# Performance work log

Hardware: AMD Instinct MI355X
Metric: run time of the kernel (lower is better)

Reference implementation:

```python
import jax, jax.numpy as jnp
import numpy as np

VOCAB, EMB, RNN, OUT = 32000, 512, 1024, 4


def setup_inputs() -> dict:
    key = jax.random.key(0)
    ks = jax.random.split(key, 8)
    stdv = 1.0 / np.sqrt(RNN)
    u = lambda k, shape, s: jax.random.uniform(k, shape, jnp.float32, -s, s)
    return {
        "x": jax.random.randint(ks[0], (512, 64), 0, VOCAB),
        "emb_table": jax.random.normal(ks[1], (VOCAB, EMB), jnp.float32),
        "w_ih": u(ks[2], (3 * RNN, EMB), stdv),
        "w_hh": u(ks[3], (3 * RNN, RNN), stdv),
        "b_ih": u(ks[4], (3 * RNN,), stdv),
        "b_hh": u(ks[5], (3 * RNN,), stdv),
        "fc_w": u(ks[6], (OUT, RNN), 1.0 / np.sqrt(RNN)),
        "fc_b": u(ks[7], (OUT,), 1.0 / np.sqrt(RNN)),
    }


def reference(x, emb_table, w_ih, w_hh, b_ih, b_hh, fc_w, fc_b):
    # x: [T, B] int indices
    T, B = x.shape
    embedded = emb_table[x]  # [T, B, EMB]
    # precompute input projections for all timesteps at once: [T, B, 3*RNN]
    gi_all = jnp.einsum('tbe,ge->tbg', embedded, w_ih) + b_ih

    def step(h, gi):
        gh = h @ w_hh.T + b_hh  # [B, 3*RNN]
        i_r, i_i, i_n = jnp.split(gi, 3, axis=1)
        h_r, h_i, h_n = jnp.split(gh, 3, axis=1)
        r = jax.nn.sigmoid(i_r + h_r)
        z = jax.nn.sigmoid(i_i + h_i)
        n = jnp.tanh(i_n + r * h_n)
        hy = z * n + (1.0 - z) * h  # note: matches GRUCellExposed (z gates newgate)
        return hy, hy

    h0 = jnp.zeros((B, w_hh.shape[1]), embedded.dtype)
    h_last, _ = jax.lax.scan(step, h0, gi_all)
    out = h_last @ fc_w.T + fc_b  # [B, OUT]
    return out
```

## Files before the change

### kernel.cpp

```cpp
#include <hip/hip_runtime.h>
#include <hip/hip_bf16.h>

typedef __attribute__((ext_vector_type(8))) short  short8;
typedef __attribute__((ext_vector_type(4))) float  f32x4;

#define T_TOTAL 512
#define BATCH   64
#define EMB     512
#define RNN     1024
#define G3      3072
#define WROWS   48
#define WPAD    1032
#define RPAD    18
#define NWG     256
#define NGRP    4
#define NLINE   2
#define SMEM_BYTES (WROWS * WPAD * 2 + 4 * WROWS * RPAD * 4)

__device__ __forceinline__ unsigned short f2bf(float f) {
    union { float f; unsigned int u; } v; v.f = f;
    unsigned int r = v.u + 0x7fffu + ((v.u >> 16) & 1u);
    return (unsigned short)(r >> 16);
}
__device__ __forceinline__ float bf2f(unsigned short h) {
    union { unsigned int u; float f; } v; v.u = ((unsigned int)h) << 16;
    return v.f;
}
__device__ __forceinline__ float sigmoidf_(float x) { return 1.f / (1.f + __expf(-x)); }
__device__ __forceinline__ float tanhf_(float x) {
    float ax = fabsf(x);
    float e2 = __expf(-2.f * ax);
    float t  = (1.f - e2) / (1.f + e2);
    return x < 0.f ? -t : t;
}

__device__ __forceinline__ void gbar_arrive(unsigned int* lines, int lid,
                                            unsigned int ph) {
    __syncthreads();
    if (threadIdx.x == 0)
        __hip_atomic_fetch_add(&lines[lid * 64], 1u,
                               __ATOMIC_RELAXED, __HIP_MEMORY_SCOPE_AGENT);
}
__device__ __forceinline__ void gbar_wait(unsigned int* lines, unsigned int ph) {
    if (threadIdx.x < NLINE) {
        while (__hip_atomic_load(&lines[threadIdx.x * 64], __ATOMIC_RELAXED,
                                 __HIP_MEMORY_SCOPE_AGENT) < ph * 32u)
            __builtin_amdgcn_s_sleep(1);
    }
    __syncthreads();
}

__global__ void bar_init(unsigned int* bar) {
    for (int i = threadIdx.x; i < NGRP * 256; i += 256) bar[i] = 0;
}

__global__ __launch_bounds__(256) void gi_kernel(
    const int* __restrict__ x, const float* __restrict__ emb,
    const float* __restrict__ w_ih, const float* __restrict__ b_ih,
    unsigned short* __restrict__ gi, int t0)
{
    __shared__ __align__(16) unsigned short Asm[128 * 40];
    __shared__ __align__(16) unsigned short Bsm[128 * 40];

    const int tid = threadIdx.x;
    const int m0 = blockIdx.x * 128;
    const int n0 = blockIdx.y * 128;

    const int r    = tid >> 1;
    const int half = tid & 1;
    const int xi = x[t0 * BATCH + m0 + r];
    const float* arow = emb  + (size_t)xi * EMB + half * 16;
    const float* brow = w_ih + (size_t)(n0 + r) * EMB + half * 16;
    unsigned short* adst = &Asm[r * 40 + half * 16];
    unsigned short* bdst = &Bsm[r * 40 + half * 16];

    const int lane = tid & 63, wv = tid >> 6;
    const int m_off = (wv & 1) * 64, n_off = (wv >> 1) * 64;
    const int lr = lane & 15, lq = lane >> 4;

    f32x4 acc[4][4];
    #pragma unroll
    for (int i = 0; i < 4; ++i)
        #pragma unroll
        for (int j = 0; j < 4; ++j) acc[i][j] = (f32x4){0.f, 0.f, 0.f, 0.f};

    for (int k0 = 0; k0 < EMB; k0 += 32) {
        const float4 a0 = *(const float4*)(arow + k0);
        const float4 a1 = *(const float4*)(arow + k0 + 4);
        const float4 a2 = *(const float4*)(arow + k0 + 8);
        const float4 a3 = *(const float4*)(arow + k0 + 12);
        const float4 b0 = *(const float4*)(brow + k0);
        const float4 b1 = *(const float4*)(brow + k0 + 4);
        const float4 b2 = *(const float4*)(brow + k0 + 8);
        const float4 b3 = *(const float4*)(brow + k0 + 12);
        __syncthreads();
        short8 av0, av1, bv0, bv1;
        av0[0]=f2bf(a0.x); av0[1]=f2bf(a0.y); av0[2]=f2bf(a0.z); av0[3]=f2bf(a0.w);
        av0[4]=f2bf(a1.x); av0[5]=f2bf(a1.y); av0[6]=f2bf(a1.z); av0[7]=f2bf(a1.w);
        av1[0]=f2bf(a2.x); av1[1]=f2bf(a2.y); av1[2]=f2bf(a2.z); av1[3]=f2bf(a2.w);
        av1[4]=f2bf(a3.x); av1[5]=f2bf(a3.y); av1[6]=f2bf(a3.z); av1[7]=f2bf(a3.w);
        bv0[0]=f2bf(b0.x); bv0[1]=f2bf(b0.y); bv0[2]=f2bf(b0.z); bv0[3]=f2bf(b0.w);
        bv0[4]=f2bf(b1.x); bv0[5]=f2bf(b1.y); bv0[6]=f2bf(b1.z); bv0[7]=f2bf(b1.w);
        bv1[0]=f2bf(b2.x); bv1[1]=f2bf(b2.y); bv1[2]=f2bf(b2.z); bv1[3]=f2bf(b2.w);
        bv1[4]=f2bf(b3.x); bv1[5]=f2bf(b3.y); bv1[6]=f2bf(b3.z); bv1[7]=f2bf(b3.w);
        *(short8*)(adst)     = av0;
        *(short8*)(adst + 8) = av1;
        *(short8*)(bdst)     = bv0;
        *(short8*)(bdst + 8) = bv1;
        __syncthreads();

        short8 fa[4], fb[4];
        #pragma unroll
        for (int i = 0; i < 4; ++i) {
            fa[i] = *(const short8*)&Asm[(m_off + i * 16 + lr) * 40 + lq * 8];
            fb[i] = *(const short8*)&Bsm[(n_off + i * 16 + lr) * 40 + lq * 8];
        }
        #pragma unroll
        for (int mi = 0; mi < 4; ++mi)
            #pragma unroll
            for (int ni = 0; ni < 4; ++ni)
                acc[mi][ni] = __builtin_amdgcn_mfma_f32_16x16x32_bf16(
                    fa[mi], fb[ni], acc[mi][ni], 0, 0, 0);
    }

    float bia[4];
    #pragma unroll
    for (int ni = 0; ni < 4; ++ni) bia[ni] = b_ih[n0 + n_off + ni * 16 + lr];
    #pragma unroll
    for (int mi = 0; mi < 4; ++mi)
        #pragma unroll
        for (int ni = 0; ni < 4; ++ni) {
            const int n = n0 + n_off + ni * 16 + lr;
            #pragma unroll
            for (int q = 0; q < 4; ++q) {
                const int m = m0 + m_off + mi * 16 + lq * 4 + q;
                gi[(size_t)m * G3 + n] = f2bf(acc[mi][ni][q] + bia[ni]);
            }
        }
}

__global__ __launch_bounds__(256, 1) void rec_kernel(
    const unsigned short* __restrict__ gi,
    const float* __restrict__ w_hh, const float* __restrict__ b_hh,
    unsigned short* __restrict__ hb0, unsigned short* __restrict__ hb1,
    float* __restrict__ hf, unsigned int* bar, int t0, int nsteps, int pbase)
{
    extern __shared__ __align__(16) char smem[];
    unsigned short* Wsm = (unsigned short*)smem;
    float (*red)[WROWS][RPAD] = (float (*)[WROWS][RPAD])(smem + WROWS * WPAD * 2);

    const int tid = threadIdx.x;
    const int wg  = blockIdx.x;
    const int grp = wg & 3, sidx = wg >> 2;
    const int b0 = grp * 16, j0 = sidx * 16;
    unsigned int* lines = &bar[grp * 256];
    const int lid = sidx & (NLINE - 1);

    #pragma unroll 4
    for (int it = 0; it < 48; ++it) {
        const int i   = it * 256 + tid;
        const int row = i >> 8;
        const int c4  = (i & 255) * 4;
        const int gate = row >> 4, uu = row & 15;
        const float4 v = *(const float4*)(w_hh + (size_t)(gate * RNN + j0 + uu) * RNN + c4);
        unsigned short* dst = &Wsm[row * WPAD + c4];
        dst[0] = f2bf(v.x); dst[1] = f2bf(v.y); dst[2] = f2bf(v.z); dst[3] = f2bf(v.w);
    }

    const int u  = tid & 15;
    const int bl = tid >> 4;
    const int j  = j0 + u;
    const int b  = b0 + bl;
    const float bhr = b_hh[j], bhi = b_hh[RNN + j], bhn = b_hh[2 * RNN + j];

    float h_reg;
    if (t0 == 0) {
        h_reg = 0.f;
        if ((u & 1) == 0)
            __hip_atomic_store((unsigned int*)&hb0[b * RNN + j], 0u,
                               __ATOMIC_RELAXED, __HIP_MEMORY_SCOPE_AGENT);
    } else {
        h_reg = hf[b * RNN + j];
    }
    gbar_arrive(lines, lid, (unsigned)(pbase + 1));

    size_t gb = (size_t)b * G3 + j0 + u;
    float gir = bf2f(gi[gb]);
    float gii = bf2f(gi[gb + RNN]);
    float gin = bf2f(gi[gb + 2 * RNN]);
    gbar_wait(lines, (unsigned)(pbase + 1));

    const int lane = tid & 63, kq = tid >> 6;
    const int lr = lane & 15, lq = lane >> 4;
    const unsigned short* wbase = Wsm + kq * 256 + lq * 8;
    const size_t hoff = ((size_t)(b0 + lr) * RNN + kq * 256 + lq * 8) >> 2;

    for (int t = 0; t < nsteps; ++t) {
        const unsigned short* hrd = (t & 1) ? hb1 : hb0;
        unsigned short*       hwr = (t & 1) ? hb0 : hb1;

        union { unsigned long long q[2]; short8 s8; } hv[8];
        const unsigned long long* hp = (const unsigned long long*)hrd + hoff;
        #pragma unroll
        for (int ks = 0; ks < 8; ++ks) {
            hv[ks].q[0] = __hip_atomic_load(hp + ks * 8,     __ATOMIC_RELAXED,
                                            __HIP_MEMORY_SCOPE_AGENT);
            hv[ks].q[1] = __hip_atomic_load(hp + ks * 8 + 1, __ATOMIC_RELAXED,
                                            __HIP_MEMORY_SCOPE_AGENT);
        }

        f32x4 acc[3];
        acc[0] = (f32x4){0.f, 0.f, 0.f, 0.f};
        acc[1] = (f32x4){0.f, 0.f, 0.f, 0.f};
        acc[2] = (f32x4){0.f, 0.f, 0.f, 0.f};
        #pragma unroll
        for (int ks = 0; ks < 8; ++ks) {
            const int k = ks * 32;
            #pragma unroll
            for (int gt = 0; gt < 3; ++gt) {
                const short8 a = *(const short8*)(wbase + (gt * 16 + lr) * WPAD + k);
                acc[gt] = __builtin_amdgcn_mfma_f32_16x16x32_bf16(a, hv[ks].s8,
                                                                  acc[gt], 0, 0, 0);
            }
        }
        #pragma unroll
        for (int gt = 0; gt < 3; ++gt)
            #pragma unroll
            for (int q = 0; q < 4; ++q)
                red[kq][gt * 16 + lq * 4 + q][lr] = acc[gt][q];
        __syncthreads();

        const float ghr = red[0][u][bl]      + red[1][u][bl]
                        + red[2][u][bl]      + red[3][u][bl];
        const float ghi = red[0][16 + u][bl] + red[1][16 + u][bl]
                        + red[2][16 + u][bl] + red[3][16 + u][bl];
        const float ghn = red[0][32 + u][bl] + red[1][32 + u][bl]
                        + red[2][32 + u][bl] + red[3][32 + u][bl];
        const float rr = sigmoidf_(gir + ghr + bhr);
        const float zz = sigmoidf_(gii + ghi + bhi);
        const float nn = tanhf_(gin + rr * (ghn + bhn));
        h_reg = zz * nn + (1.f - zz) * h_reg;

        unsigned int hvv = (unsigned int)f2bf(h_reg);
        unsigned int ovv = __shfl_xor((int)hvv, 1);
        if ((u & 1) == 0)
            __hip_atomic_store((unsigned int*)&hwr[b * RNN + j],
                               hvv | (ovv << 16), __ATOMIC_RELAXED,
                               __HIP_MEMORY_SCOPE_AGENT);

        gbar_arrive(lines, lid, (unsigned)(pbase + 2 + t));
        const int tn = (t + 1 < nsteps) ? t + 1 : t;
        gb = ((size_t)tn * BATCH + b) * G3 + j0 + u;
        const float ngr = bf2f(gi[gb]);
        const float ngi = bf2f(gi[gb + RNN]);
        const float ngn = bf2f(gi[gb + 2 * RNN]);
        gbar_wait(lines, (unsigned)(pbase + 2 + t));
        gir = ngr; gii = ngi; gin = ngn;
    }
    hf[b * RNN + j] = h_reg;
}

__global__ __launch_bounds__(256) void out_kernel(
    const float* __restrict__ hf, const float* __restrict__ fc_w,
    const float* __restrict__ fc_b, float* __restrict__ out)
{
    __shared__ float red[256];
    const int bidx = blockIdx.x, tid = threadIdx.x;
    const int o = tid & 3, seg = tid >> 2;
    const float* hp = hf   + (size_t)bidx * RNN + seg * 16;
    const float* wp = fc_w + (size_t)o * RNN + seg * 16;
    float acc = 0.f;
    #pragma unroll
    for (int i = 0; i < 16; ++i) acc += hp[i] * wp[i];
    red[tid] = acc;
    __syncthreads();
    if (tid < 4) {
        float sv = fc_b[tid];
        #pragma unroll 8
        for (int q = 0; q < 64; ++q) sv += red[q * 4 + tid];
        out[bidx * 4 + tid] = sv;
    }
}

extern "C" void kernel_launch(void* const* d_in, const int* in_sizes, int n_in,
                              void* d_out, int out_size, void* d_ws, size_t ws_size,
                              hipStream_t stream)
{
    const int*   x     = (const int*)d_in[0];
    const float* emb   = (const float*)d_in[1];
    const float* w_ih  = (const float*)d_in[2];
    const float* w_hh  = (const float*)d_in[3];
    const float* b_ih  = (const float*)d_in[4];
    const float* b_hh  = (const float*)d_in[5];
    const float* fc_w  = (const float*)d_in[6];
    const float* fc_b  = (const float*)d_in[7];
    float*       out   = (float*)d_out;

    const size_t aux = 2 * (size_t)BATCH * RNN * 2 + (size_t)BATCH * RNN * 4
                     + NGRP * 256 * 4;
    const int tch  = (ws_size >= (size_t)T_TOTAL * BATCH * G3 * 2 + aux) ? 512 : 128;
    const int nchk = T_TOTAL / tch;

    char* ws = (char*)d_ws;
    unsigned short* gi_buf = (unsigned short*)ws;
    size_t off = (size_t)tch * BATCH * G3 * 2;
    unsigned short* hb0 = (unsigned short*)(ws + off); off += (size_t)BATCH * RNN * 2;
    unsigned short* hb1 = (unsigned short*)(ws + off); off += (size_t)BATCH * RNN * 2;
    float*          hf  = (float*)(ws + off);          off += (size_t)BATCH * RNN * 4;
    unsigned int*   bar = (unsigned int*)(ws + off);

    hipFuncSetAttribute((const void*)rec_kernel,
                        hipFuncAttributeMaxDynamicSharedMemorySize, SMEM_BYTES);

    bar_init<<<dim3(1), dim3(256), 0, stream>>>(bar);

    for (int c = 0; c < nchk; ++c) {
        int t0 = c * tch, ns = tch, pb = c * (tch + 1);
        gi_kernel<<<dim3(tch * BATCH / 128, 24), dim3(256), 0, stream>>>(
            x, emb, w_ih, b_ih, gi_buf, t0);
        void* args[10];
        args[0] = (void*)&gi_buf; args[1] = (void*)&w_hh; args[2] = (void*)&b_hh;
        args[3] = (void*)&hb0;    args[4] = (void*)&hb1;  args[5] = (void*)&hf;
        args[6] = (void*)&bar;    args[7] = (void*)&t0;   args[8] = (void*)&ns;
        args[9] = (void*)&pb;
        hipLaunchCooperativeKernel((const void*)rec_kernel, dim3(NWG), dim3(256),
                                   args, SMEM_BYTES, stream);
    }
    out_kernel<<<dim3(BATCH), dim3(256), 0, stream>>>(hf, fc_w, fc_b, out);
}
```

Baseline: 2.130 ms.

## Replace per-step grid barrier with epoch-tagged hidden-state flags polled by consumers

Removes the atomic counter barrier between timesteps. Each hidden value is now stored as a 32-bit word whose upper half holds an epoch/step tag, and consumers spin on the exact h slices they need until every tag matches. This is meant to cut global barrier latency and let workgroups proceed as soon as their dependencies are ready. The reduction buffer is double-buffered so the lack of a trailing syncthreads stays safe. The cost is doubled h buffer traffic, inline-asm cache-bypassing loads, and a persistent epoch counter that must not wrap.

Result: slower. 3.000 ms (+40.9%).

```diff
diff --git a/kernel.cpp b/kernel.cpp
--- a/kernel.cpp
+++ b/kernel.cpp
@@ -3,6 +3,7 @@
 
 typedef __attribute__((ext_vector_type(8))) short  short8;
 typedef __attribute__((ext_vector_type(4))) float  f32x4;
+typedef __attribute__((ext_vector_type(4))) unsigned int u32x4;
 
 #define T_TOTAL 512
 #define BATCH   64
@@ -13,9 +14,7 @@
 #define WPAD    1032
 #define RPAD    18
 #define NWG     256
-#define NGRP    4
-#define NLINE   2
-#define SMEM_BYTES (WROWS * WPAD * 2 + 4 * WROWS * RPAD * 4)
+#define SMEM_BYTES (WROWS * WPAD * 2 + 2 * 4 * WROWS * RPAD * 4)
 
 __device__ __forceinline__ unsigned short f2bf(float f) {
     union { float f; unsigned int u; } v; v.f = f;
@@ -34,25 +33,7 @@
     return x < 0.f ? -t : t;
 }
 
-__device__ __forceinline__ void gbar_arrive(unsigned int* lines, int lid,
-                                            unsigned int ph) {
-    __syncthreads();
-    if (threadIdx.x == 0)
-        __hip_atomic_fetch_add(&lines[lid * 64], 1u,
-                               __ATOMIC_RELAXED, __HIP_MEMORY_SCOPE_AGENT);
-}
-__device__ __forceinline__ void gbar_wait(unsigned int* lines, unsigned int ph) {
-    if (threadIdx.x < NLINE) {
-        while (__hip_atomic_load(&lines[threadIdx.x * 64], __ATOMIC_RELAXED,
-                                 __HIP_MEMORY_SCOPE_AGENT) < ph * 32u)
-            __builtin_amdgcn_s_sleep(1);
-    }
-    __syncthreads();
-}
-
-__global__ void bar_init(unsigned int* bar) {
-    for (int i = threadIdx.x; i < NGRP * 256; i += 256) bar[i] = 0;
-}
+__global__ void epoch_kernel(unsigned int* ep) { if (threadIdx.x == 0) ++*ep; }
 
 __global__ __launch_bounds__(256) void gi_kernel(
     const int* __restrict__ x, const float* __restrict__ emb,
@@ -142,19 +123,21 @@
 __global__ __launch_bounds__(256, 1) void rec_kernel(
     const unsigned short* __restrict__ gi,
     const float* __restrict__ w_hh, const float* __restrict__ b_hh,
-    unsigned short* __restrict__ hb0, unsigned short* __restrict__ hb1,
-    float* __restrict__ hf, unsigned int* bar, int t0, int nsteps, int pbase)
+    unsigned int* __restrict__ hb0, unsigned int* __restrict__ hb1,
+    float* __restrict__ hf, const unsigned int* __restrict__ ep,
+    int t0, int nsteps)
 {
     extern __shared__ __align__(16) char smem[];
     unsigned short* Wsm = (unsigned short*)smem;
-    float (*red)[WROWS][RPAD] = (float (*)[WROWS][RPAD])(smem + WROWS * WPAD * 2);
+    float (*red)[4][WROWS][RPAD] =
+        (float (*)[4][WROWS][RPAD])(smem + WROWS * WPAD * 2);
 
     const int tid = threadIdx.x;
     const int wg  = blockIdx.x;
     const int grp = wg & 3, sidx = wg >> 2;
     const int b0 = grp * 16, j0 = sidx * 16;
-    unsigned int* lines = &bar[grp * 256];
-    const int lid = sidx & (NLINE - 1);
+
+    const unsigned int ebase = ep[0] * 1024u;
 
     #pragma unroll 4
     for (int it = 0; it < 48; ++it) {
@@ -176,37 +159,80 @@
     float h_reg;
     if (t0 == 0) {
         h_reg = 0.f;
-        if ((u & 1) == 0)
-            __hip_atomic_store((unsigned int*)&hb0[b * RNN + j], 0u,
-                               __ATOMIC_RELAXED, __HIP_MEMORY_SCOPE_AGENT);
+        __hip_atomic_store(&hb0[(size_t)b * RNN + j], ebase << 16,
+                           __ATOMIC_RELAXED, __HIP_MEMORY_SCOPE_AGENT);
     } else {
-        h_reg = hf[b * RNN + j];
-    }
-    gbar_arrive(lines, lid, (unsigned)(pbase + 1));
-
-    size_t gb = (size_t)b * G3 + j0 + u;
-    float gir = bf2f(gi[gb]);
-    float gii = bf2f(gi[gb + RNN]);
-    float gin = bf2f(gi[gb + 2 * RNN]);
-    gbar_wait(lines, (unsigned)(pbase + 1));
+        h_reg = hf[(size_t)b * RNN + j];
+    }
+    __syncthreads();
+
+    {
+    }
+    size_t gb0 = (size_t)b * G3 + j;
+    float gir = bf2f(gi[gb0]);
+    float gii = bf2f(gi[gb0 + RNN]);
+    float gin = bf2f(gi[gb0 + 2 * RNN]);
 
     const int lane = tid & 63, kq = tid >> 6;
     const int lr = lane & 15, lq = lane >> 4;
     const unsigned short* wbase = Wsm + kq * 256 + lq * 8;
-    const size_t hoff = ((size_t)(b0 + lr) * RNN + kq * 256 + lq * 8) >> 2;
+    const unsigned int* hpo0 = hb0 + (size_t)(b0 + lr) * RNN + kq * 256 + lq * 8;
+    const unsigned int* hpo1 = hb1 + (size_t)(b0 + lr) * RNN + kq * 256 + lq * 8;
+    unsigned int* hw0 = hb0 + (size_t)b * RNN + j;
+    unsigned int* hw1 = hb1 + (size_t)b * RNN + j;
 
     for (int t = 0; t < nsteps; ++t) {
-        const unsigned short* hrd = (t & 1) ? hb1 : hb0;
-        unsigned short*       hwr = (t & 1) ? hb0 : hb1;
-
-        union { unsigned long long q[2]; short8 s8; } hv[8];
-        const unsigned long long* hp = (const unsigned long long*)hrd + hoff;
+        const int g = t0 + t;
+        const unsigned int texp = (ebase + (unsigned)g) << 16;
+        const unsigned int* hp = (g & 1) ? hpo1 : hpo0;
+        unsigned int* hwp      = (g & 1) ? hw0  : hw1;
+
+        const int tn = (t + 1 < nsteps) ? t + 1 : t;
+        const size_t gbn = ((size_t)tn * BATCH + b) * G3 + j;
+        const float ngr = bf2f(gi[gbn]);
+        const float ngi = bf2f(gi[gbn + RNN]);
+        const float ngn = bf2f(gi[gbn + 2 * RNN]);
+
+        for (;;) {
+            unsigned int s = 0;
+            #pragma unroll
+            for (int ks = 0; ks < 8; ++ks)
+                s |= __hip_atomic_load(hp + ks * 32, __ATOMIC_RELAXED,
+                                       __HIP_MEMORY_SCOPE_AGENT) ^ texp;
+            if (__all((s & 0xFFFF0000u) == 0)) break;
+        }
+
+        u32x4 q0[8], q1[8];
+        for (;;) {
+            #pragma unroll
+            for (int ks = 0; ks < 8; ++ks) {
+                asm volatile("global_load_dwordx4 %0, %1, off sc0 sc1"
+                             : "=v"(q0[ks]) : "v"(hp + ks * 32) : "memory");
+                asm volatile("global_load_dwordx4 %0, %1, off sc0 sc1"
+                             : "=v"(q1[ks]) : "v"(hp + ks * 32 + 4) : "memory");
+            }
+            asm volatile("s_waitcnt vmcnt(0)" ::: "memory");
+            __builtin_amdgcn_sched_barrier(0);
+            unsigned int s = 0;
+            #pragma unroll
+            for (int ks = 0; ks < 8; ++ks) {
+                s |= (q0[ks].x ^ texp) | (q0[ks].y ^ texp)
+                   | (q0[ks].z ^ texp) | (q0[ks].w ^ texp);
+                s |= (q1[ks].x ^ texp) | (q1[ks].y ^ texp)
+                   | (q1[ks].z ^ texp) | (q1[ks].w ^ texp);
+            }
+            if (__all((s & 0xFFFF0000u) == 0)) break;
+        }
+
+        short8 hfrag[8];
         #pragma unroll
         for (int ks = 0; ks < 8; ++ks) {
-            hv[ks].q[0] = __hip_atomic_load(hp + ks * 8,     __ATOMIC_RELAXED,
-                                            __HIP_MEMORY_SCOPE_AGENT);
-            hv[ks].q[1] = __hip_atomic_load(hp + ks * 8 + 1, __ATOMIC_RELAXED,
-                                            __HIP_MEMORY_SCOPE_AGENT);
+            union { unsigned int d[4]; short8 s8; } pk;
+            pk.d[0] = __builtin_amdgcn_perm(q0[ks].y, q0[ks].x, 0x05040100u);
+            pk.d[1] = __builtin_amdgcn_perm(q0[ks].w, q0[ks].z, 0x05040100u);
+            pk.d[2] = __builtin_amdgcn_perm(q1[ks].y, q1[ks].x, 0x05040100u);
+            pk.d[3] = __builtin_amdgcn_perm(q1[ks].w, q1[ks].z, 0x05040100u);
+            hfrag[ks] = pk.s8;
         }
 
         f32x4 acc[3];
@@ -219,45 +245,34 @@
             #pragma unroll
             for (int gt = 0; gt < 3; ++gt) {
                 const short8 a = *(const short8*)(wbase + (gt * 16 + lr) * WPAD + k);
-                acc[gt] = __builtin_amdgcn_mfma_f32_16x16x32_bf16(a, hv[ks].s8,
+                acc[gt] = __builtin_amdgcn_mfma_f32_16x16x32_bf16(a, hfrag[ks],
                                                                   acc[gt], 0, 0, 0);
             }
         }
+        float (*rcur)[WROWS][RPAD] = red[t & 1];
         #pragma unroll
         for (int gt = 0; gt < 3; ++gt)
             #pragma unroll
             for (int q = 0; q < 4; ++q)
-                red[kq][gt * 16 + lq * 4 + q][lr] = acc[gt][q];
+                rcur[kq][gt * 16 + lq * 4 + q][lr] = acc[gt][q];
         __syncthreads();
 
-        const float ghr = red[0][u][bl]      + red[1][u][bl]
-                        + red[2][u][bl]      + red[3][u][bl];
-        const float ghi = red[0][16 + u][bl] + red[1][16 + u][bl]
-                        + red[2][16 + u][bl] + red[3][16 + u][bl];
-        const float ghn = red[0][32 + u][bl] + red[1][32 + u][bl]
-                        + red[2][32 + u][bl] + red[3][32 + u][bl];
+        const float ghr = rcur[0][u][bl]      + rcur[1][u][bl]
+                        + rcur[2][u][bl]      + rcur[3][u][bl];
+        const float ghi = rcur[0][16 + u][bl] + rcur[1][16 + u][bl]
+                        + rcur[2][16 + u][bl] + rcur[3][16 + u][bl];
+        const float ghn = rcur[0][32 + u][bl] + rcur[1][32 + u][bl]
+                        + rcur[2][32 + u][bl] + rcur[3][32 + u][bl];
         const float rr = sigmoidf_(gir + ghr + bhr);
         const float zz = sigmoidf_(gii + ghi + bhi);
         const float nn = tanhf_(gin + rr * (ghn + bhn));
         h_reg = zz * nn + (1.f - zz) * h_reg;
 
-        unsigned int hvv = (unsigned int)f2bf(h_reg);
-        unsigned int ovv = __shfl_xor((int)hvv, 1);
-        if ((u & 1) == 0)
-            __hip_atomic_store((unsigned int*)&hwr[b * RNN + j],
-                               hvv | (ovv << 16), __ATOMIC_RELAXED,
-                               __HIP_MEMORY_SCOPE_AGENT);
-
-        gbar_arrive(lines, lid, (unsigned)(pbase + 2 + t));
-        const int tn = (t + 1 < nsteps) ? t + 1 : t;
-        gb = ((size_t)tn * BATCH + b) * G3 + j0 + u;
-        const float ngr = bf2f(gi[gb]);
-        const float ngi = bf2f(gi[gb + RNN]);
-        const float ngn = bf2f(gi[gb + 2 * RNN]);
-        gbar_wait(lines, (unsigned)(pbase + 2 + t));
+        __hip_atomic_store(hwp, (texp + 0x10000u) | (unsigned)f2bf(h_reg),
+                           __ATOMIC_RELAXED, __HIP_MEMORY_SCOPE_AGENT);
         gir = ngr; gii = ngi; gin = ngn;
     }
-    hf[b * RNN + j] = h_reg;
+    hf[(size_t)b * RNN + j] = h_reg;
 }
 
 __global__ __launch_bounds__(256) void out_kernel(
@@ -296,33 +311,31 @@
     const float* fc_b  = (const float*)d_in[7];
     float*       out   = (float*)d_out;
 
-    const size_t aux = 2 * (size_t)BATCH * RNN * 2 + (size_t)BATCH * RNN * 4
-                     + NGRP * 256 * 4;
+    const size_t aux = 3 * (size_t)BATCH * RNN * 4 + 256;
     const int tch  = (ws_size >= (size_t)T_TOTAL * BATCH * G3 * 2 + aux) ? 512 : 128;
     const int nchk = T_TOTAL / tch;
 
     char* ws = (char*)d_ws;
     unsigned short* gi_buf = (unsigned short*)ws;
     size_t off = (size_t)tch * BATCH * G3 * 2;
-    unsigned short* hb0 = (unsigned short*)(ws + off); off += (size_t)BATCH * RNN * 2;
-    unsigned short* hb1 = (unsigned short*)(ws + off); off += (size_t)BATCH * RNN * 2;
-    float*          hf  = (float*)(ws + off);          off += (size_t)BATCH * RNN * 4;
-    unsigned int*   bar = (unsigned int*)(ws + off);
+    unsigned int* hb0 = (unsigned int*)(ws + off); off += (size_t)BATCH * RNN * 4;
+    unsigned int* hb1 = (unsigned int*)(ws + off); off += (size_t)BATCH * RNN * 4;
+    float*        hf  = (float*)(ws + off);        off += (size_t)BATCH * RNN * 4;
+    unsigned int* ep  = (unsigned int*)(ws + off);
 
     hipFuncSetAttribute((const void*)rec_kernel,
                         hipFuncAttributeMaxDynamicSharedMemorySize, SMEM_BYTES);
 
-    bar_init<<<dim3(1), dim3(256), 0, stream>>>(bar);
+    epoch_kernel<<<dim3(1), dim3(1), 0, stream>>>(ep);
 
     for (int c = 0; c < nchk; ++c) {
-        int t0 = c * tch, ns = tch, pb = c * (tch + 1);
+        int t0 = c * tch, ns = tch;
         gi_kernel<<<dim3(tch * BATCH / 128, 24), dim3(256), 0, stream>>>(
             x, emb, w_ih, b_ih, gi_buf, t0);
-        void* args[10];
+        void* args[9];
         args[0] = (void*)&gi_buf; args[1] = (void*)&w_hh; args[2] = (void*)&b_hh;
         args[3] = (void*)&hb0;    args[4] = (void*)&hb1;  args[5] = (void*)&hf;
-        args[6] = (void*)&bar;    args[7] = (void*)&t0;   args[8] = (void*)&ns;
-        args[9] = (void*)&pb;
+        args[6] = (void*)&ep;     args[7] = (void*)&t0;   args[8] = (void*)&ns;
         hipLaunchCooperativeKernel((const void*)rec_kernel, dim3(NWG), dim3(256),
                                    args, SMEM_BYTES, stream);
     }
```

## Split grid barrier into per-k-quarter lines and pre-convert GEMM inputs to bf16

Applied to the files above, without the earlier changes.

The recurrent kernel's group barrier changes from two shared counters, which every block waited on, to four counters indexed by the block's j-quarter. Each wave polls only the counter for the quarter of h it reads, and waves proceed independently without a block-wide syncthreads after the wait, which should shorten the per-step barrier latency. Separately, when workspace allows, the embedding table and w_ih are converted to bf16 up front so the input-projection GEMM loads half the bytes and skips per-tile conversion. The cost is converting the whole 32000x512 embedding table, most of which is never gathered, and the per-wave waits add memory-ordering risk.

New measurement: 2.286 ms. +7.3%, slower.

```diff
diff --git a/kernel.cpp b/kernel.cpp
--- a/kernel.cpp
+++ b/kernel.cpp
@@ -6,6 +6,7 @@
 
 #define T_TOTAL 512
 #define BATCH   64
+#define VOCAB   32000
 #define EMB     512
 #define RNN     1024
 #define G3      3072
@@ -14,7 +15,7 @@
 #define RPAD    18
 #define NWG     256
 #define NGRP    4
-#define NLINE   2
+#define NLINE   4
 #define SMEM_BYTES (WROWS * WPAD * 2 + 4 * WROWS * RPAD * 4)
 
 __device__ __forceinline__ unsigned short f2bf(float f) {
@@ -34,29 +35,27 @@
     return x < 0.f ? -t : t;
 }
 
-__device__ __forceinline__ void gbar_arrive(unsigned int* lines, int lid,
-                                            unsigned int ph) {
-    __syncthreads();
-    if (threadIdx.x == 0)
-        __hip_atomic_fetch_add(&lines[lid * 64], 1u,
-                               __ATOMIC_RELAXED, __HIP_MEMORY_SCOPE_AGENT);
-}
-__device__ __forceinline__ void gbar_wait(unsigned int* lines, unsigned int ph) {
-    if (threadIdx.x < NLINE) {
-        while (__hip_atomic_load(&lines[threadIdx.x * 64], __ATOMIC_RELAXED,
-                                 __HIP_MEMORY_SCOPE_AGENT) < ph * 32u)
-            __builtin_amdgcn_s_sleep(1);
-    }
-    __syncthreads();
-}
-
 __global__ void bar_init(unsigned int* bar) {
     for (int i = threadIdx.x; i < NGRP * 256; i += 256) bar[i] = 0;
 }
 
+__global__ __launch_bounds__(256) void cvt_bf16_kernel(
+    const float* __restrict__ s, unsigned short* __restrict__ d, int n8)
+{
+    const int i = blockIdx.x * 256 + threadIdx.x;
+    if (i >= n8) return;
+    const float4 a = ((const float4*)s)[i * 2];
+    const float4 b = ((const float4*)s)[i * 2 + 1];
+    short8 v;
+    v[0] = f2bf(a.x); v[1] = f2bf(a.y); v[2] = f2bf(a.z); v[3] = f2bf(a.w);
+    v[4] = f2bf(b.x); v[5] = f2bf(b.y); v[6] = f2bf(b.z); v[7] = f2bf(b.w);
+    ((short8*)d)[i] = v;
+}
+
+template<bool BF>
 __global__ __launch_bounds__(256) void gi_kernel(
-    const int* __restrict__ x, const float* __restrict__ emb,
-    const float* __restrict__ w_ih, const float* __restrict__ b_ih,
+    const int* __restrict__ x, const void* __restrict__ embp,
+    const void* __restrict__ wihp, const float* __restrict__ b_ih,
     unsigned short* __restrict__ gi, int t0)
 {
     __shared__ __align__(16) unsigned short Asm[128 * 40];
@@ -69,8 +68,6 @@
     const int r    = tid >> 1;
     const int half = tid & 1;
     const int xi = x[t0 * BATCH + m0 + r];
-    const float* arow = emb  + (size_t)xi * EMB + half * 16;
-    const float* brow = w_ih + (size_t)(n0 + r) * EMB + half * 16;
     unsigned short* adst = &Asm[r * 40 + half * 16];
     unsigned short* bdst = &Bsm[r * 40 + half * 16];
 
@@ -84,43 +81,77 @@
         #pragma unroll
         for (int j = 0; j < 4; ++j) acc[i][j] = (f32x4){0.f, 0.f, 0.f, 0.f};
 
-    for (int k0 = 0; k0 < EMB; k0 += 32) {
-        const float4 a0 = *(const float4*)(arow + k0);
-        const float4 a1 = *(const float4*)(arow + k0 + 4);
-        const float4 a2 = *(const float4*)(arow + k0 + 8);
-        const float4 a3 = *(const float4*)(arow + k0 + 12);
-        const float4 b0 = *(const float4*)(brow + k0);
-        const float4 b1 = *(const float4*)(brow + k0 + 4);
-        const float4 b2 = *(const float4*)(brow + k0 + 8);
-        const float4 b3 = *(const float4*)(brow + k0 + 12);
-        __syncthreads();
-        short8 av0, av1, bv0, bv1;
-        av0[0]=f2bf(a0.x); av0[1]=f2bf(a0.y); av0[2]=f2bf(a0.z); av0[3]=f2bf(a0.w);
-        av0[4]=f2bf(a1.x); av0[5]=f2bf(a1.y); av0[6]=f2bf(a1.z); av0[7]=f2bf(a1.w);
-        av1[0]=f2bf(a2.x); av1[1]=f2bf(a2.y); av1[2]=f2bf(a2.z); av1[3]=f2bf(a2.w);
-        av1[4]=f2bf(a3.x); av1[5]=f2bf(a3.y); av1[6]=f2bf(a3.z); av1[7]=f2bf(a3.w);
-        bv0[0]=f2bf(b0.x); bv0[1]=f2bf(b0.y); bv0[2]=f2bf(b0.z); bv0[3]=f2bf(b0.w);
-        bv0[4]=f2bf(b1.x); bv0[5]=f2bf(b1.y); bv0[6]=f2bf(b1.z); bv0[7]=f2bf(b1.w);
-        bv1[0]=f2bf(b2.x); bv1[1]=f2bf(b2.y); bv1[2]=f2bf(b2.z); bv1[3]=f2bf(b2.w);
-        bv1[4]=f2bf(b3.x); bv1[5]=f2bf(b3.y); bv1[6]=f2bf(b3.z); bv1[7]=f2bf(b3.w);
-        *(short8*)(adst)     = av0;
-        *(short8*)(adst + 8) = av1;
-        *(short8*)(bdst)     = bv0;
-        *(short8*)(bdst + 8) = bv1;
-        __syncthreads();
-
-        short8 fa[4], fb[4];
-        #pragma unroll
-        for (int i = 0; i < 4; ++i) {
-            fa[i] = *(const short8*)&Asm[(m_off + i * 16 + lr) * 40 + lq * 8];
-            fb[i] = *(const short8*)&Bsm[(n_off + i * 16 + lr) * 40 + lq * 8];
-        }
-        #pragma unroll
-        for (int mi = 0; mi < 4; ++mi)
-            #pragma unroll
-            for (int ni = 0; ni < 4; ++ni)
-                acc[mi][ni] = __builtin_amdgcn_mfma_f32_16x16x32_bf16(
-                    fa[mi], fb[ni], acc[mi][ni], 0, 0, 0);
+    if constexpr (BF) {
+        const unsigned short* arow = (const unsigned short*)embp
+                                   + (size_t)xi * EMB + half * 16;
+        const unsigned short* brow = (const unsigned short*)wihp
+                                   + (size_t)(n0 + r) * EMB + half * 16;
+        for (int k0 = 0; k0 < EMB; k0 += 32) {
+            const short8 av0 = *(const short8*)(arow + k0);
+            const short8 av1 = *(const short8*)(arow + k0 + 8);
+            const short8 bv0 = *(const short8*)(brow + k0);
+            const short8 bv1 = *(const short8*)(brow + k0 + 8);
+            __syncthreads();
+            *(short8*)(adst)     = av0;
+            *(short8*)(adst + 8) = av1;
+            *(short8*)(bdst)     = bv0;
+            *(short8*)(bdst + 8) = bv1;
+            __syncthreads();
+
+            short8 fa[4], fb[4];
+            #pragma unroll
+            for (int i = 0; i < 4; ++i) {
+                fa[i] = *(const short8*)&Asm[(m_off + i * 16 + lr) * 40 + lq * 8];
+                fb[i] = *(const short8*)&Bsm[(n_off + i * 16 + lr) * 40 + lq * 8];
+            }
+            #pragma unroll
+            for (int mi = 0; mi < 4; ++mi)
+                #pragma unroll
+                for (int ni = 0; ni < 4; ++ni)
+                    acc[mi][ni] = __builtin_amdgcn_mfma_f32_16x16x32_bf16(
+                        fa[mi], fb[ni], acc[mi][ni], 0, 0, 0);
+        }
+    } else {
+        const float* arow = (const float*)embp + (size_t)xi * EMB + half * 16;
+        const float* brow = (const float*)wihp + (size_t)(n0 + r) * EMB + half * 16;
+        for (int k0 = 0; k0 < EMB; k0 += 32) {
+            const float4 a0 = *(const float4*)(arow + k0);
+            const float4 a1 = *(const float4*)(arow + k0 + 4);
+            const float4 a2 = *(const float4*)(arow + k0 + 8);
+            const float4 a3 = *(const float4*)(arow + k0 + 12);
+            const float4 b0 = *(const float4*)(brow + k0);
+            const float4 b1 = *(const float4*)(brow + k0 + 4);
+            const float4 b2 = *(const float4*)(brow + k0 + 8);
+            const float4 b3 = *(const float4*)(brow + k0 + 12);
+            __syncthreads();
+            short8 av0, av1, bv0, bv1;
+            av0[0]=f2bf(a0.x); av0[1]=f2bf(a0.y); av0[2]=f2bf(a0.z); av0[3]=f2bf(a0.w);
+            av0[4]=f2bf(a1.x); av0[5]=f2bf(a1.y); av0[6]=f2bf(a1.z); av0[7]=f2bf(a1.w);
+            av1[0]=f2bf(a2.x); av1[1]=f2bf(a2.y); av1[2]=f2bf(a2.z); av1[3]=f2bf(a2.w);
+            av1[4]=f2bf(a3.x); av1[5]=f2bf(a3.y); av1[6]=f2bf(a3.z); av1[7]=f2bf(a3.w);
+            bv0[0]=f2bf(b0.x); bv0[1]=f2bf(b0.y); bv0[2]=f2bf(b0.z); bv0[3]=f2bf(b0.w);
+            bv0[4]=f2bf(b1.x); bv0[5]=f2bf(b1.y); bv0[6]=f2bf(b1.z); bv0[7]=f2bf(b1.w);
+            bv1[0]=f2bf(b2.x); bv1[1]=f2bf(b2.y); bv1[2]=f2bf(b2.z); bv1[3]=f2bf(b2.w);
+            bv1[4]=f2bf(b3.x); bv1[5]=f2bf(b3.y); bv1[6]=f2bf(b3.z); bv1[7]=f2bf(b3.w);
+            *(short8*)(adst)     = av0;
+            *(short8*)(adst + 8) = av1;
+            *(short8*)(bdst)     = bv0;
+            *(short8*)(bdst + 8) = bv1;
+            __syncthreads();
+
+            short8 fa[4], fb[4];
+            #pragma unroll
+            for (int i = 0; i < 4; ++i) {
+                fa[i] = *(const short8*)&Asm[(m_off + i * 16 + lr) * 40 + lq * 8];
+                fb[i] = *(const short8*)&Bsm[(n_off + i * 16 + lr) * 40 + lq * 8];
+            }
+            #pragma unroll
+            for (int mi = 0; mi < 4; ++mi)
+                #pragma unroll
+                for (int ni = 0; ni < 4; ++ni)
+                    acc[mi][ni] = __builtin_amdgcn_mfma_f32_16x16x32_bf16(
+                        fa[mi], fb[ni], acc[mi][ni], 0, 0, 0);
+        }
     }
 
     float bia[4];
@@ -154,7 +185,7 @@
     const int grp = wg & 3, sidx = wg >> 2;
     const int b0 = grp * 16, j0 = sidx * 16;
     unsigned int* lines = &bar[grp * 256];
-    const int lid = sidx & (NLINE - 1);
+    const int qw = sidx >> 4;
 
     #pragma unroll 4
     for (int it = 0; it < 48; ++it) {
@@ -182,18 +213,29 @@
     } else {
         h_reg = hf[b * RNN + j];
     }
-    gbar_arrive(lines, lid, (unsigned)(pbase + 1));
+    __syncthreads();
+    if (tid == 0)
+        __hip_atomic_fetch_add(&lines[qw * 64], 1u,
+                               __ATOMIC_RELAXED, __HIP_MEMORY_SCOPE_AGENT);
 
     size_t gb = (size_t)b * G3 + j0 + u;
     float gir = bf2f(gi[gb]);
     float gii = bf2f(gi[gb + RNN]);
     float gin = bf2f(gi[gb + 2 * RNN]);
-    gbar_wait(lines, (unsigned)(pbase + 1));
 
     const int lane = tid & 63, kq = tid >> 6;
     const int lr = lane & 15, lq = lane >> 4;
     const unsigned short* wbase = Wsm + kq * 256 + lq * 8;
     const size_t hoff = ((size_t)(b0 + lr) * RNN + kq * 256 + lq * 8) >> 2;
+    unsigned int* myline = &lines[kq * 64];
+
+    if (lane == 0) {
+        while (__hip_atomic_load(myline, __ATOMIC_RELAXED,
+                                 __HIP_MEMORY_SCOPE_AGENT)
+               < (unsigned)(pbase + 1) * 16u)
+            __builtin_amdgcn_s_sleep(1);
+    }
+    asm volatile("" ::: "memory");
 
     for (int t = 0; t < nsteps; ++t) {
         const unsigned short* hrd = (t & 1) ? hb1 : hb0;
@@ -248,13 +290,24 @@
                                hvv | (ovv << 16), __ATOMIC_RELAXED,
                                __HIP_MEMORY_SCOPE_AGENT);
 
-        gbar_arrive(lines, lid, (unsigned)(pbase + 2 + t));
+        __syncthreads();
+        if (tid == 0)
+            __hip_atomic_fetch_add(&lines[qw * 64], 1u,
+                                   __ATOMIC_RELAXED, __HIP_MEMORY_SCOPE_AGENT);
+
         const int tn = (t + 1 < nsteps) ? t + 1 : t;
         gb = ((size_t)tn * BATCH + b) * G3 + j0 + u;
         const float ngr = bf2f(gi[gb]);
         const float ngi = bf2f(gi[gb + RNN]);
         const float ngn = bf2f(gi[gb + 2 * RNN]);
-        gbar_wait(lines, (unsigned)(pbase + 2 + t));
+
+        if (lane == 0) {
+            while (__hip_atomic_load(myline, __ATOMIC_RELAXED,
+                                     __HIP_MEMORY_SCOPE_AGENT)
+                   < (unsigned)(pbase + 2 + t) * 16u)
+                __builtin_amdgcn_s_sleep(1);
+        }
+        asm volatile("" ::: "memory");
         gir = ngr; gii = ngi; gin = ngn;
     }
     hf[b * RNN + j] = h_reg;
@@ -298,7 +351,12 @@
 
     const size_t aux = 2 * (size_t)BATCH * RNN * 2 + (size_t)BATCH * RNN * 4
                      + NGRP * 256 * 4;
-    const int tch  = (ws_size >= (size_t)T_TOTAL * BATCH * G3 * 2 + aux) ? 512 : 128;
+    const size_t gi_full  = (size_t)T_TOTAL * BATCH * G3 * 2;
+    const size_t embbf_b  = (size_t)VOCAB * EMB * 2;
+    const size_t wihbf_b  = (size_t)G3 * EMB * 2;
+    const bool fused  = ws_size >= gi_full + aux;
+    const bool bfpath = ws_size >= gi_full + aux + embbf_b + wihbf_b;
+    const int tch  = fused ? 512 : 128;
     const int nchk = T_TOTAL / tch;
 
     char* ws = (char*)d_ws;
@@ -307,17 +365,29 @@
     unsigned short* hb0 = (unsigned short*)(ws + off); off += (size_t)BATCH * RNN * 2;
     unsigned short* hb1 = (unsigned short*)(ws + off); off += (size_t)BATCH * RNN * 2;
     float*          hf  = (float*)(ws + off);          off += (size_t)BATCH * RNN * 4;
-    unsigned int*   bar = (unsigned int*)(ws + off);
+    unsigned int*   bar = (unsigned int*)(ws + off);   off += NGRP * 256 * 4;
+    unsigned short* embbf = (unsigned short*)(ws + off); off += embbf_b;
+    unsigned short* wihbf = (unsigned short*)(ws + off);
 
     hipFuncSetAttribute((const void*)rec_kernel,
                         hipFuncAttributeMaxDynamicSharedMemorySize, SMEM_BYTES);
 
     bar_init<<<dim3(1), dim3(256), 0, stream>>>(bar);
+    if (bfpath) {
+        cvt_bf16_kernel<<<dim3((VOCAB * EMB / 8 + 255) / 256), dim3(256), 0, stream>>>(
+            emb, embbf, VOCAB * EMB / 8);
+        cvt_bf16_kernel<<<dim3((G3 * EMB / 8 + 255) / 256), dim3(256), 0, stream>>>(
+            w_ih, wihbf, G3 * EMB / 8);
+    }
 
     for (int c = 0; c < nchk; ++c) {
         int t0 = c * tch, ns = tch, pb = c * (tch + 1);
-        gi_kernel<<<dim3(tch * BATCH / 128, 24), dim3(256), 0, stream>>>(
-            x, emb, w_ih, b_ih, gi_buf, t0);
+        if (bfpath)
+            gi_kernel<true><<<dim3(tch * BATCH / 128, 24), dim3(256), 0, stream>>>(
+                x, (const void*)embbf, (const void*)wihbf, b_ih, gi_buf, t0);
+        else
+            gi_kernel<false><<<dim3(tch * BATCH / 128, 24), dim3(256), 0, stream>>>(
+                x, (const void*)emb, (const void*)w_ih, b_ih, gi_buf, t0);
         void* args[10];
         args[0] = (void*)&gi_buf; args[1] = (void*)&w_hh; args[2] = (void*)&b_hh;
         args[3] = (void*)&hb0;    args[4] = (void*)&hb1;  args[5] = (void*)&hf;
```

## Fuse input projection into persistent GRU recurrence kernel, drop gi buffer

Applied to the files above, without the earlier changes.

Removes the separate gi GEMM kernel and its large bf16 gi workspace. Each persistent workgroup now holds its slice of w_ih in LDS and computes the next step's input projection with MFMA while it waits at the grid barrier. Optionally pre-converts the embedding table to bf16 in workspace so per-step gathers load half the bytes. This adds per-step MFMA work and an extra __syncthreads inside the latency-critical recurrence loop, and raises LDS use.

Measured after the change: 2.227 ms. 4.6% more time.

```diff
diff --git a/kernel.cpp b/kernel.cpp
--- a/kernel.cpp
+++ b/kernel.cpp
@@ -6,16 +6,18 @@
 
 #define T_TOTAL 512
 #define BATCH   64
+#define VOCAB   32000
 #define EMB     512
 #define RNN     1024
 #define G3      3072
 #define WROWS   48
 #define WPAD    1032
+#define APAD2   520
 #define RPAD    18
 #define NWG     256
 #define NGRP    4
 #define NLINE   2
-#define SMEM_BYTES (WROWS * WPAD * 2 + 4 * WROWS * RPAD * 4)
+#define REC_SMEM (WROWS * WPAD * 2 + WROWS * APAD2 * 2 + 4 * WROWS * RPAD * 4)
 
 __device__ __forceinline__ unsigned short f2bf(float f) {
     union { float f; unsigned int u; } v; v.f = f;
@@ -54,100 +56,32 @@
     for (int i = threadIdx.x; i < NGRP * 256; i += 256) bar[i] = 0;
 }
 
-__global__ __launch_bounds__(256) void gi_kernel(
-    const int* __restrict__ x, const float* __restrict__ emb,
+__global__ __launch_bounds__(256) void cvt_bf16_kernel(
+    const float* __restrict__ s, unsigned short* __restrict__ d, int n8)
+{
+    const int i = blockIdx.x * 256 + threadIdx.x;
+    if (i >= n8) return;
+    const float4 a = ((const float4*)s)[i * 2];
+    const float4 b = ((const float4*)s)[i * 2 + 1];
+    short8 v;
+    v[0] = f2bf(a.x); v[1] = f2bf(a.y); v[2] = f2bf(a.z); v[3] = f2bf(a.w);
+    v[4] = f2bf(b.x); v[5] = f2bf(b.y); v[6] = f2bf(b.z); v[7] = f2bf(b.w);
+    ((short8*)d)[i] = v;
+}
+
+template<bool BF>
+__global__ __launch_bounds__(256, 1) void rec_kernel(
+    const int* __restrict__ x, const void* __restrict__ embp,
     const float* __restrict__ w_ih, const float* __restrict__ b_ih,
-    unsigned short* __restrict__ gi, int t0)
-{
-    __shared__ __align__(16) unsigned short Asm[128 * 40];
-    __shared__ __align__(16) unsigned short Bsm[128 * 40];
-
-    const int tid = threadIdx.x;
-    const int m0 = blockIdx.x * 128;
-    const int n0 = blockIdx.y * 128;
-
-    const int r    = tid >> 1;
-    const int half = tid & 1;
-    const int xi = x[t0 * BATCH + m0 + r];
-    const float* arow = emb  + (size_t)xi * EMB + half * 16;
-    const float* brow = w_ih + (size_t)(n0 + r) * EMB + half * 16;
-    unsigned short* adst = &Asm[r * 40 + half * 16];
-    unsigned short* bdst = &Bsm[r * 40 + half * 16];
-
-    const int lane = tid & 63, wv = tid >> 6;
-    const int m_off = (wv & 1) * 64, n_off = (wv >> 1) * 64;
-    const int lr = lane & 15, lq = lane >> 4;
-
-    f32x4 acc[4][4];
-    #pragma unroll
-    for (int i = 0; i < 4; ++i)
-        #pragma unroll
-        for (int j = 0; j < 4; ++j) acc[i][j] = (f32x4){0.f, 0.f, 0.f, 0.f};
-
-    for (int k0 = 0; k0 < EMB; k0 += 32) {
-        const float4 a0 = *(const float4*)(arow + k0);
-        const float4 a1 = *(const float4*)(arow + k0 + 4);
-        const float4 a2 = *(const float4*)(arow + k0 + 8);
-        const float4 a3 = *(const float4*)(arow + k0 + 12);
-        const float4 b0 = *(const float4*)(brow + k0);
-        const float4 b1 = *(const float4*)(brow + k0 + 4);
-        const float4 b2 = *(const float4*)(brow + k0 + 8);
-        const float4 b3 = *(const float4*)(brow + k0 + 12);
-        __syncthreads();
-        short8 av0, av1, bv0, bv1;
-        av0[0]=f2bf(a0.x); av0[1]=f2bf(a0.y); av0[2]=f2bf(a0.z); av0[3]=f2bf(a0.w);
-        av0[4]=f2bf(a1.x); av0[5]=f2bf(a1.y); av0[6]=f2bf(a1.z); av0[7]=f2bf(a1.w);
-        av1[0]=f2bf(a2.x); av1[1]=f2bf(a2.y); av1[2]=f2bf(a2.z); av1[3]=f2bf(a2.w);
-        av1[4]=f2bf(a3.x); av1[5]=f2bf(a3.y); av1[6]=f2bf(a3.z); av1[7]=f2bf(a3.w);
-        bv0[0]=f2bf(b0.x); bv0[1]=f2bf(b0.y); bv0[2]=f2bf(b0.z); bv0[3]=f2bf(b0.w);
-        bv0[4]=f2bf(b1.x); bv0[5]=f2bf(b1.y); bv0[6]=f2bf(b1.z); bv0[7]=f2bf(b1.w);
-        bv1[0]=f2bf(b2.x); bv1[1]=f2bf(b2.y); bv1[2]=f2bf(b2.z); bv1[3]=f2bf(b2.w);
-        bv1[4]=f2bf(b3.x); bv1[5]=f2bf(b3.y); bv1[6]=f2bf(b3.z); bv1[7]=f2bf(b3.w);
-        *(short8*)(adst)     = av0;
-        *(short8*)(adst + 8) = av1;
-        *(short8*)(bdst)     = bv0;
-        *(short8*)(bdst + 8) = bv1;
-        __syncthreads();
-
-        short8 fa[4], fb[4];
-        #pragma unroll
-        for (int i = 0; i < 4; ++i) {
-            fa[i] = *(const short8*)&Asm[(m_off + i * 16 + lr) * 40 + lq * 8];
-            fb[i] = *(const short8*)&Bsm[(n_off + i * 16 + lr) * 40 + lq * 8];
-        }
-        #pragma unroll
-        for (int mi = 0; mi < 4; ++mi)
-            #pragma unroll
-            for (int ni = 0; ni < 4; ++ni)
-                acc[mi][ni] = __builtin_amdgcn_mfma_f32_16x16x32_bf16(
-                    fa[mi], fb[ni], acc[mi][ni], 0, 0, 0);
-    }
-
-    float bia[4];
-    #pragma unroll
-    for (int ni = 0; ni < 4; ++ni) bia[ni] = b_ih[n0 + n_off + ni * 16 + lr];
-    #pragma unroll
-    for (int mi = 0; mi < 4; ++mi)
-        #pragma unroll
-        for (int ni = 0; ni < 4; ++ni) {
-            const int n = n0 + n_off + ni * 16 + lr;
-            #pragma unroll
-            for (int q = 0; q < 4; ++q) {
-                const int m = m0 + m_off + mi * 16 + lq * 4 + q;
-                gi[(size_t)m * G3 + n] = f2bf(acc[mi][ni][q] + bia[ni]);
-            }
-        }
-}
-
-__global__ __launch_bounds__(256, 1) void rec_kernel(
-    const unsigned short* __restrict__ gi,
     const float* __restrict__ w_hh, const float* __restrict__ b_hh,
     unsigned short* __restrict__ hb0, unsigned short* __restrict__ hb1,
     float* __restrict__ hf, unsigned int* bar, int t0, int nsteps, int pbase)
 {
     extern __shared__ __align__(16) char smem[];
     unsigned short* Wsm = (unsigned short*)smem;
-    float (*red)[WROWS][RPAD] = (float (*)[WROWS][RPAD])(smem + WROWS * WPAD * 2);
+    unsigned short* Wih = (unsigned short*)smem + WROWS * WPAD;
+    float (*red)[WROWS][RPAD] =
+        (float (*)[WROWS][RPAD])(smem + WROWS * WPAD * 2 + WROWS * APAD2 * 2);
 
     const int tid = threadIdx.x;
     const int wg  = blockIdx.x;
@@ -166,12 +100,23 @@
         unsigned short* dst = &Wsm[row * WPAD + c4];
         dst[0] = f2bf(v.x); dst[1] = f2bf(v.y); dst[2] = f2bf(v.z); dst[3] = f2bf(v.w);
     }
+    #pragma unroll 4
+    for (int it = 0; it < 24; ++it) {
+        const int i   = it * 256 + tid;
+        const int row = i >> 7;
+        const int c4  = (i & 127) * 4;
+        const int gate = row >> 4, uu = row & 15;
+        const float4 v = *(const float4*)(w_ih + (size_t)(gate * RNN + j0 + uu) * EMB + c4);
+        unsigned short* dst = &Wih[row * APAD2 + c4];
+        dst[0] = f2bf(v.x); dst[1] = f2bf(v.y); dst[2] = f2bf(v.z); dst[3] = f2bf(v.w);
+    }
 
     const int u  = tid & 15;
     const int bl = tid >> 4;
     const int j  = j0 + u;
     const int b  = b0 + bl;
-    const float bhr = b_hh[j], bhi = b_hh[RNN + j], bhn = b_hh[2 * RNN + j];
+    const float bhr  = b_hh[j], bhi  = b_hh[RNN + j], bhn  = b_hh[2 * RNN + j];
+    const float bihr = b_ih[j], bihi = b_ih[RNN + j], bihn = b_ih[2 * RNN + j];
 
     float h_reg;
     if (t0 == 0) {
@@ -184,18 +129,64 @@
     }
     gbar_arrive(lines, lid, (unsigned)(pbase + 1));
 
-    size_t gb = (size_t)b * G3 + j0 + u;
-    float gir = bf2f(gi[gb]);
-    float gii = bf2f(gi[gb + RNN]);
-    float gin = bf2f(gi[gb + 2 * RNN]);
-    gbar_wait(lines, (unsigned)(pbase + 1));
-
     const int lane = tid & 63, kq = tid >> 6;
     const int lr = lane & 15, lq = lane >> 4;
-    const unsigned short* wbase = Wsm + kq * 256 + lq * 8;
+    const unsigned short* wbase  = Wsm + kq * 256 + lq * 8;
+    const unsigned short* wibase = Wih + kq * 128 + lq * 8;
     const size_t hoff = ((size_t)(b0 + lr) * RNN + kq * 256 + lq * 8) >> 2;
 
+    auto gi_compute = [&](int tg) {
+        const int xi = x[tg * BATCH + b0 + lr];
+        short8 bfr[4];
+        if constexpr (BF) {
+            const unsigned short* erow = (const unsigned short*)embp
+                                       + (size_t)xi * EMB + kq * 128 + lq * 8;
+            #pragma unroll
+            for (int ks = 0; ks < 4; ++ks)
+                bfr[ks] = *(const short8*)(erow + ks * 32);
+        } else {
+            const float* erow = (const float*)embp
+                              + (size_t)xi * EMB + kq * 128 + lq * 8;
+            #pragma unroll
+            for (int ks = 0; ks < 4; ++ks) {
+                const float4 e0 = *(const float4*)(erow + ks * 32);
+                const float4 e1 = *(const float4*)(erow + ks * 32 + 4);
+                short8 v;
+                v[0]=f2bf(e0.x); v[1]=f2bf(e0.y); v[2]=f2bf(e0.z); v[3]=f2bf(e0.w);
+                v[4]=f2bf(e1.x); v[5]=f2bf(e1.y); v[6]=f2bf(e1.z); v[7]=f2bf(e1.w);
+                bfr[ks] = v;
+            }
+        }
+        f32x4 acc2[3];
+        acc2[0] = (f32x4){0.f, 0.f, 0.f, 0.f};
+        acc2[1] = (f32x4){0.f, 0.f, 0.f, 0.f};
+        acc2[2] = (f32x4){0.f, 0.f, 0.f, 0.f};
+        #pragma unroll
+        for (int ks = 0; ks < 4; ++ks)
+            #pragma unroll
+            for (int gt = 0; gt < 3; ++gt) {
+                const short8 a = *(const short8*)(wibase + (gt * 16 + lr) * APAD2 + ks * 32);
+                acc2[gt] = __builtin_amdgcn_mfma_f32_16x16x32_bf16(a, bfr[ks],
+                                                                   acc2[gt], 0, 0, 0);
+            }
+        #pragma unroll
+        for (int gt = 0; gt < 3; ++gt)
+            #pragma unroll
+            for (int q = 0; q < 4; ++q)
+                red[kq][gt * 16 + lq * 4 + q][lr] = acc2[gt][q];
+    };
+
+    gi_compute(t0);
+    gbar_wait(lines, (unsigned)(pbase + 1));
+
     for (int t = 0; t < nsteps; ++t) {
+        const float gir = red[0][u][bl]      + red[1][u][bl]
+                        + red[2][u][bl]      + red[3][u][bl]      + bihr;
+        const float gii = red[0][16 + u][bl] + red[1][16 + u][bl]
+                        + red[2][16 + u][bl] + red[3][16 + u][bl] + bihi;
+        const float gin = red[0][32 + u][bl] + red[1][32 + u][bl]
+                        + red[2][32 + u][bl] + red[3][32 + u][bl] + bihn;
+
         const unsigned short* hrd = (t & 1) ? hb1 : hb0;
         unsigned short*       hwr = (t & 1) ? hb0 : hb1;
 
@@ -223,6 +214,7 @@
                                                                   acc[gt], 0, 0, 0);
             }
         }
+        __syncthreads();
         #pragma unroll
         for (int gt = 0; gt < 3; ++gt)
             #pragma unroll
@@ -250,12 +242,8 @@
 
         gbar_arrive(lines, lid, (unsigned)(pbase + 2 + t));
         const int tn = (t + 1 < nsteps) ? t + 1 : t;
-        gb = ((size_t)tn * BATCH + b) * G3 + j0 + u;
-        const float ngr = bf2f(gi[gb]);
-        const float ngi = bf2f(gi[gb + RNN]);
-        const float ngn = bf2f(gi[gb + 2 * RNN]);
+        gi_compute(t0 + tn);
         gbar_wait(lines, (unsigned)(pbase + 2 + t));
-        gir = ngr; gii = ngi; gin = ngn;
     }
     hf[b * RNN + j] = h_reg;
 }
@@ -296,35 +284,43 @@
     const float* fc_b  = (const float*)d_in[7];
     float*       out   = (float*)d_out;
 
-    const size_t aux = 2 * (size_t)BATCH * RNN * 2 + (size_t)BATCH * RNN * 4
-                     + NGRP * 256 * 4;
-    const int tch  = (ws_size >= (size_t)T_TOTAL * BATCH * G3 * 2 + aux) ? 512 : 128;
-    const int nchk = T_TOTAL / tch;
+    const size_t bar_b   = (size_t)NGRP * 256 * 4;
+    const size_t base_b  = 2 * (size_t)BATCH * RNN * 2
+                         + (size_t)BATCH * RNN * 4 + bar_b;
+    const size_t embbf_b = (size_t)VOCAB * EMB * 2;
+    const bool bfpath = ws_size >= base_b + embbf_b;
 
     char* ws = (char*)d_ws;
-    unsigned short* gi_buf = (unsigned short*)ws;
-    size_t off = (size_t)tch * BATCH * G3 * 2;
+    size_t off = 0;
     unsigned short* hb0 = (unsigned short*)(ws + off); off += (size_t)BATCH * RNN * 2;
     unsigned short* hb1 = (unsigned short*)(ws + off); off += (size_t)BATCH * RNN * 2;
     float*          hf  = (float*)(ws + off);          off += (size_t)BATCH * RNN * 4;
-    unsigned int*   bar = (unsigned int*)(ws + off);
-
-    hipFuncSetAttribute((const void*)rec_kernel,
-                        hipFuncAttributeMaxDynamicSharedMemorySize, SMEM_BYTES);
+    unsigned int*   bar = (unsigned int*)(ws + off);   off += bar_b;
+    unsigned short* embbf = (unsigned short*)(ws + off);
+
+    hipFuncSetAttribute((const void*)rec_kernel<true>,
+                        hipFuncAttributeMaxDynamicSharedMemorySize, REC_SMEM);
+    hipFuncSetAttribute((const void*)rec_kernel<false>,
+                        hipFuncAttributeMaxDynamicSharedMemorySize, REC_SMEM);
 
     bar_init<<<dim3(1), dim3(256), 0, stream>>>(bar);
-
-    for (int c = 0; c < nchk; ++c) {
-        int t0 = c * tch, ns = tch, pb = c * (tch + 1);
-        gi_kernel<<<dim3(tch * BATCH / 128, 24), dim3(256), 0, stream>>>(
-            x, emb, w_ih, b_ih, gi_buf, t0);
-        void* args[10];
-        args[0] = (void*)&gi_buf; args[1] = (void*)&w_hh; args[2] = (void*)&b_hh;
-        args[3] = (void*)&hb0;    args[4] = (void*)&hb1;  args[5] = (void*)&hf;
-        args[6] = (void*)&bar;    args[7] = (void*)&t0;   args[8] = (void*)&ns;
-        args[9] = (void*)&pb;
-        hipLaunchCooperativeKernel((const void*)rec_kernel, dim3(NWG), dim3(256),
-                                   args, SMEM_BYTES, stream);
-    }
+    if (bfpath)
+        cvt_bf16_kernel<<<dim3((VOCAB * EMB / 8 + 255) / 256), dim3(256), 0, stream>>>(
+            emb, embbf, VOCAB * EMB / 8);
+
+    int t0 = 0, ns = T_TOTAL, pb = 0;
+    const void* embp = bfpath ? (const void*)embbf : (const void*)emb;
+    void* args[13];
+    args[0]  = (void*)&x;    args[1]  = (void*)&embp;  args[2]  = (void*)&w_ih;
+    args[3]  = (void*)&b_ih; args[4]  = (void*)&w_hh;  args[5]  = (void*)&b_hh;
+    args[6]  = (void*)&hb0;  args[7]  = (void*)&hb1;   args[8]  = (void*)&hf;
+    args[9]  = (void*)&bar;  args[10] = (void*)&t0;    args[11] = (void*)&ns;
+    args[12] = (void*)&pb;
+    if (bfpath)
+        hipLaunchCooperativeKernel((const void*)rec_kernel<true>, dim3(NWG), dim3(256),
+                                   args, REC_SMEM, stream);
+    else
+        hipLaunchCooperativeKernel((const void*)rec_kernel<false>, dim3(NWG), dim3(256),
+                                   args, REC_SMEM, stream);
     out_kernel<<<dim3(BATCH), dim3(256), 0, stream>>>(hf, fc_w, fc_b, out);
 }
```
